# Kernel optimization log

Measured on AMD Instinct MI355X. Metric: run time of the kernel, lower is better.

The kernel has to match this reference:

```python
import jax, jax.numpy as jnp
import numpy as np

THETA = 10000.0
NUM_HEADS = 16
MAX_SEQ_LEN = 2048

def _rope_tables(d_k, max_seq_len, theta=THETA):
    dims = jnp.arange(0, d_k, 2, dtype=jnp.float32)
    freqs = 1.0 / theta ** (dims / d_k)
    t = jnp.arange(max_seq_len, dtype=jnp.float32)
    angles = jnp.outer(t, freqs)  # (max_seq_len, d_k//2)
    return jnp.cos(angles), jnp.sin(angles)

def _apply_rope(x, token_positions, cos_tab, sin_tab):
    # x: (..., seq_len, d_k)
    cos = jnp.repeat(cos_tab[token_positions], 2, axis=-1)  # (seq_len, d_k)
    sin = jnp.repeat(sin_tab[token_positions], 2, axis=-1)
    # interleaved rotate-half: (-x1, x0, -x3, x2, ...)
    xp = x.reshape(*x.shape[:-1], -1, 2)
    x_neg = jnp.stack([-xp[..., 1], xp[..., 0]], axis=-1).reshape(x.shape)
    return x * cos + x_neg * sin

def setup_inputs() -> dict:
    key = jax.random.key(0)
    ks = jax.random.split(key, 5)
    B, S, D = 4, 2048, 1024
    scale = 1.0 / np.sqrt(D)
    return {
        "x": jax.random.normal(ks[0], (B, S, D), dtype=jnp.float32),
        "q_proj": jax.random.normal(ks[1], (D, D), dtype=jnp.float32) * scale,
        "k_proj": jax.random.normal(ks[2], (D, D), dtype=jnp.float32) * scale,
        "v_proj": jax.random.normal(ks[3], (D, D), dtype=jnp.float32) * scale,
        "o_proj": jax.random.normal(ks[4], (D, D), dtype=jnp.float32) * scale,
        "token_positions": jnp.arange(S, dtype=jnp.int64),
    }

def reference(x, q_proj, k_proj, v_proj, o_proj, token_positions):
    B, S, D = x.shape
    H = NUM_HEADS
    d_k = D // H
    cos_tab, sin_tab = _rope_tables(d_k, MAX_SEQ_LEN)

    q = (x @ q_proj).reshape(B, S, H, d_k).transpose(0, 2, 1, 3)  # (B,H,S,d_k)
    k = (x @ k_proj).reshape(B, S, H, d_k).transpose(0, 2, 1, 3)
    v = (x @ v_proj).reshape(B, S, H, d_k).transpose(0, 2, 1, 3)

    q = _apply_rope(q, token_positions, cos_tab, sin_tab)
    k = _apply_rope(k, token_positions, cos_tab, sin_tab)

    scores = jnp.einsum('bhqd,bhkd->bhqk', q, k) / jnp.sqrt(jnp.float32(d_k))
    causal = jnp.tril(jnp.ones((S, S), dtype=bool))
    scores = jnp.where(causal, scores, -jnp.inf)
    attn = jax.nn.softmax(scores, axis=-1)
    out = jnp.einsum('bhqk,bhkd->bhqd', attn, v)  # (B,H,S,d_k)
    out = out.transpose(0, 2, 1, 3).reshape(B, S, D)
    return out @ o_proj
```

## Files before the change

kernel.cpp:

```cpp
#include <hip/hip_runtime.h>
#include <hip/hip_bf16.h>
#include <stdint.h>


typedef __attribute__((ext_vector_type(8))) short short8;
typedef __attribute__((ext_vector_type(4))) float floatx4;
typedef __attribute__((ext_vector_type(16))) float floatx16;

#define MFMA16(a,b,c) __builtin_amdgcn_mfma_f32_16x16x32_bf16((a),(b),(c),0,0,0)
#define MFMA32(a,b,c) __builtin_amdgcn_mfma_f32_32x32x16_bf16((a),(b),(c),0,0,0)

__device__ __forceinline__ uint32_t fbits(float f){ uint32_t u; __builtin_memcpy(&u,&f,4); return u; }
__device__ __forceinline__ unsigned short f2bf(float f) {
    uint32_t u = fbits(f);
    return (unsigned short)((u + 0x7fffu + ((u>>16)&1u)) >> 16);
}
__device__ __forceinline__ float bf2f(unsigned short s){ uint32_t u = (uint32_t)s<<16; float f; __builtin_memcpy(&f,&u,4); return f; }
__device__ __forceinline__ uint32_t pkbf(float lo, float hi) {
#if __has_builtin(__builtin_amdgcn_cvt_pk_bf16_f32)
    auto r = __builtin_amdgcn_cvt_pk_bf16_f32(lo, hi);
    uint32_t u; __builtin_memcpy(&u, &r, sizeof(u));
    return u;
#else
    return __builtin_amdgcn_perm(fbits(hi)+0x8000u, fbits(lo)+0x8000u, 0x07060302u);
#endif
}

__device__ __forceinline__ void load_lds16(const unsigned short* g, unsigned short* l) {
    __builtin_amdgcn_global_load_lds(
        (const __attribute__((address_space(1))) void*)g,
        (__attribute__((address_space(3))) void*)l, 16, 0, 0);
}

__device__ __forceinline__ bool sniff_f32(const unsigned short* xr) {
    int lane = threadIdx.x & 63;
    int bad = 0;
#pragma unroll
    for (int i = 0; i < 16; i++) {
        float v = bf2f(xr[lane * 16 + i]);
        if (!(__builtin_fabsf(v) < 1e10f)) bad = 1;
    }
    return __ballot(bad != 0) != 0ull;
}

__global__ __launch_bounds__(256) void prep_k(
    const void* __restrict__ x,
    const void* __restrict__ wq, const void* __restrict__ wk,
    const void* __restrict__ wv, const void* __restrict__ wo,
    unsigned short* __restrict__ WT, unsigned short* __restrict__ WoT,
    float2* __restrict__ tab, unsigned short* __restrict__ xb) {
    int blk = blockIdx.x, t = threadIdx.x;
    bool f32 = sniff_f32((const unsigned short*)x);
    if (blk < 4096) {
        __shared__ unsigned short tile[32][33];
        int mat = blk >> 10, r = blk & 1023;
        const void* src = (mat == 0) ? wq : (mat == 1) ? wk : (mat == 2) ? wv : wo;
        unsigned short* dst = (mat < 3) ? (WT + (size_t)mat * 1048576) : WoT;
        int bx = (r & 31) * 32, by = (r >> 5) * 32;
        int tx = t & 31, ty = t >> 5;
#pragma unroll
        for (int j = 0; j < 32; j += 8) {
            size_t idx = (size_t)(by + ty + j) * 1024 + bx + tx;
            float v = f32 ? ((const float*)src)[idx] : bf2f(((const unsigned short*)src)[idx]);
            tile[ty + j][tx] = f2bf(v);
        }
        __syncthreads();
#pragma unroll
        for (int j = 0; j < 32; j += 8)
            dst[(size_t)(bx + ty + j) * 1024 + by + tx] = tile[tx][ty + j];
    } else if (blk < 4352) {
        int i = (blk - 4096) * 256 + t;
        int pos = i >> 5, j = i & 31;
        float freq = exp2f(-(float)(2 * j) * (1.0f / 64.0f) * 13.287712379549449f);
        float a = (float)pos * freq;
        tab[i] = make_float2(cosf(a), sinf(a));
    } else {
        size_t base = (size_t)(blk - 4352) * 2048 + (size_t)t * 8;
        if (f32) {
            const float4* s4 = (const float4*)((const float*)x + base);
            float4 a = s4[0], b = s4[1];
            uint4 o;
            o.x = pkbf(a.x, a.y); o.y = pkbf(a.z, a.w);
            o.z = pkbf(b.x, b.y); o.w = pkbf(b.z, b.w);
            *(uint4*)(xb + base) = o;
        } else {
            *(uint4*)(xb + base) = *(const uint4*)((const unsigned short*)x + base);
        }
    }
}

template <int MODE>
__global__ __launch_bounds__(256) void gemm_bt(
    const unsigned short* __restrict__ A,
    const unsigned short* __restrict__ Bt,
    void* __restrict__ C0,
    unsigned short* __restrict__ C1,
    unsigned short* __restrict__ C2,
    const float2* __restrict__ tab,
    const unsigned short* __restrict__ xsniff) {
    const int K = 1024;
    __shared__ __align__(16) unsigned short Al[2][128 * 32];
    __shared__ __align__(16) unsigned short Bl[2][128 * 32];

    int m0 = blockIdx.y * 128;
    int n0 = blockIdx.x * 128;
    int t = threadIdx.x;
    int lane = t & 63, w = t >> 6;
    int quad = lane >> 4, l15 = lane & 15;
    int wm = (w >> 1) * 64, wn = (w & 1) * 64;

    floatx4 acc[4][4];
#pragma unroll
    for (int i = 0; i < 4; i++)
#pragma unroll
        for (int j = 0; j < 4; j++) acc[i][j] = (floatx4){0.f, 0.f, 0.f, 0.f};

    const unsigned short* ag[2];
    const unsigned short* bg[2];
    int lofs[2];
#pragma unroll
    for (int c = 0; c < 2; c++) {
        int row = w * 32 + c * 16 + (lane >> 2);
        ag[c] = A + (size_t)(m0 + row) * K + (lane & 3) * 8;
        bg[c] = Bt + (size_t)(n0 + row) * K + (lane & 3) * 8;
        lofs[c] = (w * 32 + c * 16) * 32;
    }

#pragma unroll
    for (int c = 0; c < 2; c++) {
        load_lds16(ag[c], &Al[0][lofs[c]]);
        load_lds16(bg[c], &Bl[0][lofs[c]]);
        ag[c] += 32; bg[c] += 32;
    }
    asm volatile("s_waitcnt vmcnt(0)" ::: "memory");
    __syncthreads();

    for (int kk = 0; kk < 16; kk++) {
#pragma unroll
        for (int c = 0; c < 2; c++) {
            load_lds16(ag[c], &Al[1][lofs[c]]);
            load_lds16(bg[c], &Bl[1][lofs[c]]);
            ag[c] += 32; bg[c] += 32;
        }
        {
            short8 af[4], bfr[4];
#pragma unroll
            for (int i = 0; i < 4; i++)
                af[i] = *(const short8*)&Al[0][(wm + i * 16 + l15) * 32 + quad * 8];
#pragma unroll
            for (int j = 0; j < 4; j++)
                bfr[j] = *(const short8*)&Bl[0][(wn + j * 16 + l15) * 32 + quad * 8];
#pragma unroll
            for (int i = 0; i < 4; i++)
#pragma unroll
                for (int j = 0; j < 4; j++) acc[i][j] = MFMA16(af[i], bfr[j], acc[i][j]);
        }
        asm volatile("s_waitcnt vmcnt(0)" ::: "memory");
        __syncthreads();

        if (kk < 15) {
#pragma unroll
            for (int c = 0; c < 2; c++) {
                load_lds16(ag[c], &Al[0][lofs[c]]);
                load_lds16(bg[c], &Bl[0][lofs[c]]);
                ag[c] += 32; bg[c] += 32;
            }
        }
        {
            short8 af[4], bfr[4];
#pragma unroll
            for (int i = 0; i < 4; i++)
                af[i] = *(const short8*)&Al[1][(wm + i * 16 + l15) * 32 + quad * 8];
#pragma unroll
            for (int j = 0; j < 4; j++)
                bfr[j] = *(const short8*)&Bl[1][(wn + j * 16 + l15) * 32 + quad * 8];
#pragma unroll
            for (int i = 0; i < 4; i++)
#pragma unroll
                for (int j = 0; j < 4; j++) acc[i][j] = MFMA16(af[i], bfr[j], acc[i][j]);
        }
        asm volatile("s_waitcnt vmcnt(0)" ::: "memory");
        __syncthreads();
    }

    bool out_f32 = (MODE == 0) ? sniff_f32(xsniff) : false;
#pragma unroll
    for (int i = 0; i < 4; i++) {
#pragma unroll
        for (int j = 0; j < 4; j++) {
            int col = n0 + wn + j * 16 + l15;
            int row0 = m0 + wm + i * 16 + quad * 4;
            if (MODE == 0) {
#pragma unroll
                for (int r = 0; r < 4; r++) {
                    size_t idx = (size_t)(row0 + r) * 1024 + col;
                    if (out_f32) ((float*)C0)[idx] = acc[i][j][r];
                    else ((unsigned short*)C0)[idx] = f2bf(acc[i][j][r]);
                }
            } else {
                int which = col >> 10, nn = col & 1023;
                int b = row0 >> 11, s0 = row0 & 2047;
                if (which == 2) {
                    int hh = nn >> 6, d = nn & 63;
                    uint32_t lo = pkbf(acc[i][j][0], acc[i][j][1]);
                    uint32_t hi = pkbf(acc[i][j][2], acc[i][j][3]);
                    *(uint64_t*)(C2 + ((size_t)((b * 16 + hh) * 64 + d)) * 2048 + s0) =
                        (uint64_t)lo | ((uint64_t)hi << 32);
                } else {
                    int d = nn & 63;
                    unsigned short* dst = (which == 0) ? (unsigned short*)C0 : C1;
                    float sc = (which == 0) ? 0.18033688011112042f : 1.0f;
#pragma unroll
                    for (int r = 0; r < 4; r++) {
                        int s = s0 + r;
                        float v = acc[i][j][r];
                        float pv = __shfl_xor(v, 1);
                        float2 cs = tab[(s << 5) + (d >> 1)];
                        float o = (d & 1) ? (v * cs.x + pv * cs.y) : (v * cs.x - pv * cs.y);
                        dst[((size_t)(b * 2048 + s)) * 1024 + nn] = f2bf(o * sc);
                    }
                }
            }
        }
    }
}

__global__ __launch_bounds__(256, 4) void flash_k(
    const unsigned short* __restrict__ Qb,
    const unsigned short* __restrict__ Kb,
    const unsigned short* __restrict__ Vt,
    unsigned short* __restrict__ A2) {
    __shared__ __align__(16) unsigned short Kl[2][64 * 64];
    __shared__ __align__(16) unsigned short Vl[2][64 * 64];

    int bh = blockIdx.x;
    int y = blockIdx.y;
    int qt = (y < 8) ? (15 - y) : (y - 8);
    int b = bh >> 4, h = bh & 15;
    int t = threadIdx.x, lane = t & 63, w = t >> 6;
    int l31 = lane & 31, half = lane >> 5;
    size_t base = ((size_t)b * 2048) * 1024 + h * 64;
    int q0w = qt * 128 + w * 32;

    short8 Qf[4];
#pragma unroll
    for (int ks = 0; ks < 4; ks++)
        Qf[ks] = *(const short8*)(Qb + base + (size_t)(q0w + l31) * 1024 + ks * 16 + half * 8);

    floatx16 O[2];
    O[0] = (floatx16)0.0f; O[1] = (floatx16)0.0f;
    float lsum = 0.f;

    int nk = 2 * (qt + 1);

    int srow = t >> 2;
    const unsigned short* kg = Kb + base + (size_t)srow * 1024 + (t & 3) * 16;
    const unsigned short* vg = Vt + ((size_t)(bh * 64 + srow)) * 2048 + (t & 3) * 16;
    int sw0 = srow * 64 + ((((t & 3) * 2 + 0) ^ (srow & 7)) * 8);
    int sw1 = srow * 64 + ((((t & 3) * 2 + 1) ^ (srow & 7)) * 8);

    short8 rk0 = *(const short8*)(kg);
    short8 rk1 = *(const short8*)(kg + 8);
    short8 rv0 = *(const short8*)(vg);
    short8 rv1 = *(const short8*)(vg + 8);

    for (int kt = 0; kt < nk; kt++) {
        int k0 = kt * 64, bf = kt & 1;
        *(short8*)&Kl[bf][sw0] = rk0;
        *(short8*)&Kl[bf][sw1] = rk1;
        *(short8*)&Vl[bf][sw0] = rv0;
        *(short8*)&Vl[bf][sw1] = rv1;
        __syncthreads();
        if (kt + 1 < nk) {
            size_t ko = (size_t)(kt + 1) * 64;
            rk0 = *(const short8*)(kg + ko * 1024);
            rk1 = *(const short8*)(kg + ko * 1024 + 8);
            rv0 = *(const short8*)(vg + ko);
            rv1 = *(const short8*)(vg + ko + 8);
        }
#pragma unroll
        for (int mb = 0; mb < 2; mb++) {
            if (k0 + mb * 32 >= q0w + 32) continue;
            short8 Ka[4];
#pragma unroll
            for (int ks = 0; ks < 4; ks++)
                Ka[ks] = *(const short8*)&Kl[bf][(mb * 32 + l31) * 64 +
                                                 (((ks * 2 + half) ^ (l31 & 7)) * 8)];
            floatx16 Sc = (floatx16)0.0f;
#pragma unroll
            for (int ks = 0; ks < 4; ks++)
                Sc = MFMA32(Ka[ks], Qf[ks], Sc);

            bool domask = (k0 + mb * 32 + 31 > q0w);
            float p[16];
#pragma unroll
            for (int e = 0; e < 16; e++) {
                float v = exp2f(Sc[e]);
                if (domask) {
                    int kv = k0 + mb * 32 + (e & 3) + ((e >> 2) << 3) + half * 4;
                    int qq = q0w + l31;
                    v = (kv > qq) ? 0.f : v;
                }
                p[e] = v;
            }
            float t0 = (p[0] + p[1]) + (p[2] + p[3]);
            float t1 = (p[4] + p[5]) + (p[6] + p[7]);
            float t2 = (p[8] + p[9]) + (p[10] + p[11]);
            float t3 = (p[12] + p[13]) + (p[14] + p[15]);
            lsum += (t0 + t1) + (t2 + t3);
            uint32_t pkm[8];
#pragma unroll
            for (int jj = 0; jj < 8; jj++)
                pkm[jj] = pkbf(p[2 * jj], p[2 * jj + 1]);

            short8 Va[2][2];
#pragma unroll
            for (int db = 0; db < 2; db++)
#pragma unroll
                for (int ks2 = 0; ks2 < 2; ks2++)
                    Va[db][ks2] = *(const short8*)&Vl[bf][(db * 32 + l31) * 64 +
                                                         ((((mb * 2 + ks2) * 2 + half) ^ (l31 & 7)) * 8)];
#pragma unroll
            for (int ks2 = 0; ks2 < 2; ks2++) {
                uint32_t p0 = pkm[4 * ks2 + 0];
                uint32_t p1 = pkm[4 * ks2 + 1];
                uint32_t p2 = pkm[4 * ks2 + 2];
                uint32_t p3 = pkm[4 * ks2 + 3];
                uint32_t u = half ? p0 : p2;
                uint32_t v2 = half ? p1 : p3;
                uint32_t ya = (uint32_t)__shfl_xor((int)u, 32);
                uint32_t yb = (uint32_t)__shfl_xor((int)v2, 32);
                union { short8 s; uint32_t q[4]; } bb;
                bb.q[0] = half ? ya : p0;
                bb.q[1] = half ? yb : p1;
                bb.q[2] = half ? p2 : ya;
                bb.q[3] = half ? p3 : yb;
#pragma unroll
                for (int db = 0; db < 2; db++)
                    O[db] = MFMA32(Va[db][ks2], bb.s, O[db]);
            }
        }
    }

    float tot = lsum + __shfl_xor(lsum, 32);
    float inv = 1.0f / tot;
#pragma unroll
    for (int db = 0; db < 2; db++) {
        int scol = q0w + l31;
        unsigned short* op = A2 + base + (size_t)scol * 1024;
#pragma unroll
        for (int g = 0; g < 4; g++) {
            int d0 = db * 32 + half * 4 + g * 8;
            float v0 = O[db][g * 4 + 0] * inv;
            float v1 = O[db][g * 4 + 1] * inv;
            float v2 = O[db][g * 4 + 2] * inv;
            float v3 = O[db][g * 4 + 3] * inv;
            uint32_t lo = pkbf(v0, v1), hi = pkbf(v2, v3);
            *(uint64_t*)(op + d0) = (uint64_t)lo | ((uint64_t)hi << 32);
        }
    }
}

extern "C" void kernel_launch(void* const* d_in, const int* in_sizes, int n_in,
                              void* d_out, int out_size, void* d_ws, size_t ws_size,
                              hipStream_t stream) {
    const void* x  = d_in[0];
    const void* wq = d_in[1];
    const void* wk = d_in[2];
    const void* wv = d_in[3];
    const void* wo = d_in[4];

    char* ws = (char*)d_ws;
    unsigned short* WT  = (unsigned short*)(ws);
    unsigned short* WoT = (unsigned short*)(ws + 6291456);
    float2*         tab = (float2*)(ws + 8388608);
    unsigned short* xb  = (unsigned short*)(ws + 8913920);
    unsigned short* Qb  = (unsigned short*)(ws + 8913920 + 16777216ull);
    unsigned short* Kb  = (unsigned short*)(ws + 8913920 + 2ull * 16777216);
    unsigned short* Vt  = (unsigned short*)(ws + 8913920 + 3ull * 16777216);
    unsigned short* A2  = xb;

    prep_k<<<8448, 256, 0, stream>>>(x, wq, wk, wv, wo, WT, WoT, tab, xb);

    gemm_bt<1><<<dim3(24, 64), 256, 0, stream>>>(xb, WT, Qb, Kb, Vt, tab,
                                                 (const unsigned short*)x);
    flash_k<<<dim3(64, 16), 256, 0, stream>>>(Qb, Kb, Vt, A2);
    gemm_bt<0><<<dim3(8, 64), 256, 0, stream>>>(A2, WoT, d_out, nullptr, nullptr, tab,
                                                (const unsigned short*)x);
}
```

Measured before the change: 281.1 us.

## Rewrite projection GEMMs with 8-wave 128x256 tiles and triple-buffered LDS pipeline

Replaces the 256-thread 128x128 double-buffered GEMM with a 512-thread 128x256 tile kernel. It uses BK=64, a three-stage LDS ring in dynamic shared memory, XOR-swizzled LDS layout, and an XCD-aware block index swizzle. Global loads for stage k+2 are interleaved between MFMA phases, with s_setprio raising MFMA priority and partial vmcnt waits. This targets better latency hiding and cache reuse in the QKV and output projections, at the cost of 144KB of LDS per block, which limits occupancy, and more barriers per k-step.

```diff
diff --git a/kernel.cpp b/kernel.cpp
--- a/kernel.cpp
+++ b/kernel.cpp
@@ -9,6 +9,9 @@
 
 #define MFMA16(a,b,c) __builtin_amdgcn_mfma_f32_16x16x32_bf16((a),(b),(c),0,0,0)
 #define MFMA32(a,b,c) __builtin_amdgcn_mfma_f32_32x32x16_bf16((a),(b),(c),0,0,0)
+#define BAR() __builtin_amdgcn_s_barrier()
+#define LGKM0 asm volatile("s_waitcnt lgkmcnt(0)" ::: "memory")
+#define VMCNT6 asm volatile("s_waitcnt vmcnt(6)" ::: "memory")
 
 __device__ __forceinline__ uint32_t fbits(float f){ uint32_t u; __builtin_memcpy(&u,&f,4); return u; }
 __device__ __forceinline__ unsigned short f2bf(float f) {
@@ -90,7 +93,7 @@
 }
 
 template <int MODE>
-__global__ __launch_bounds__(256) void gemm_bt(
+__global__ __launch_bounds__(512, 2) void gemm8(
     const unsigned short* __restrict__ A,
     const unsigned short* __restrict__ Bt,
     void* __restrict__ C0,
@@ -99,15 +102,21 @@
     const float2* __restrict__ tab,
     const unsigned short* __restrict__ xsniff) {
     const int K = 1024;
-    __shared__ __align__(16) unsigned short Al[2][128 * 32];
-    __shared__ __align__(16) unsigned short Bl[2][128 * 32];
-
-    int m0 = blockIdx.y * 128;
-    int n0 = blockIdx.x * 128;
+    extern __shared__ __align__(16) char smraw[];
+    unsigned short* Asm = (unsigned short*)smraw;
+    unsigned short* Bsm = Asm + 3 * 8192;
+
     int t = threadIdx.x;
     int lane = t & 63, w = t >> 6;
     int quad = lane >> 4, l15 = lane & 15;
-    int wm = (w >> 1) * 64, wn = (w & 1) * 64;
+    int wm = (w >> 2) * 64, wn = (w & 3) * 64;
+
+    int nbx = gridDim.x;
+    int flat = blockIdx.y * nbx + blockIdx.x;
+    int cpx = (nbx * gridDim.y) >> 3;
+    int swzid = (flat & 7) * cpx + (flat >> 3);
+    int bx = swzid % nbx, by = swzid / nbx;
+    int m0 = by * 128, n0 = bx * 256;
 
     floatx4 acc[4][4];
 #pragma unroll
@@ -115,72 +124,105 @@
 #pragma unroll
         for (int j = 0; j < 4; j++) acc[i][j] = (floatx4){0.f, 0.f, 0.f, 0.f};
 
-    const unsigned short* ag[2];
-    const unsigned short* bg[2];
-    int lofs[2];
-#pragma unroll
-    for (int c = 0; c < 2; c++) {
-        int row = w * 32 + c * 16 + (lane >> 2);
-        ag[c] = A + (size_t)(m0 + row) * K + (lane & 3) * 8;
-        bg[c] = Bt + (size_t)(n0 + row) * K + (lane & 3) * 8;
-        lofs[c] = (w * 32 + c * 16) * 32;
-    }
-
-#pragma unroll
-    for (int c = 0; c < 2; c++) {
-        load_lds16(ag[c], &Al[0][lofs[c]]);
-        load_lds16(bg[c], &Bl[0][lofs[c]]);
-        ag[c] += 32; bg[c] += 32;
-    }
-    asm volatile("s_waitcnt vmcnt(0)" ::: "memory");
+    int srow = t >> 3;
+    int sg = ((t & 7) ^ (srow & 7)) * 8;
+    const unsigned short* gA = A + (size_t)(m0 + srow) * K + sg;
+    const unsigned short* gB = Bt + (size_t)(n0 + srow) * K + sg;
+    unsigned short* lA = Asm + w * 512;
+    unsigned short* lB = Bsm + w * 512;
+
+    int rA[4], rB[4], ce[2];
+#pragma unroll
+    for (int m = 0; m < 4; m++) rA[m] = (wm + m * 16 + l15) * 64;
+#pragma unroll
+    for (int n = 0; n < 4; n++) rB[n] = (wn + n * 16 + l15) * 64;
+#pragma unroll
+    for (int ks = 0; ks < 2; ks++)
+        ce[ks] = ((ks * 64 + quad * 16) ^ ((l15 & 7) << 4)) >> 1;
+
+#pragma unroll
+    for (int kt = 0; kt < 2; kt++) {
+#pragma unroll
+        for (int h = 0; h < 2; h++)
+            load_lds16(gA + (size_t)h * 64 * K + kt * 64, lA + kt * 8192 + h * 4096);
+#pragma unroll
+        for (int c = 0; c < 4; c++)
+            load_lds16(gB + (size_t)c * 64 * K + kt * 64, lB + kt * 16384 + c * 4096);
+    }
+    VMCNT6;
     __syncthreads();
 
-    for (int kk = 0; kk < 16; kk++) {
-#pragma unroll
-        for (int c = 0; c < 2; c++) {
-            load_lds16(ag[c], &Al[1][lofs[c]]);
-            load_lds16(bg[c], &Bl[1][lofs[c]]);
-            ag[c] += 32; bg[c] += 32;
-        }
-        {
-            short8 af[4], bfr[4];
-#pragma unroll
-            for (int i = 0; i < 4; i++)
-                af[i] = *(const short8*)&Al[0][(wm + i * 16 + l15) * 32 + quad * 8];
-#pragma unroll
-            for (int j = 0; j < 4; j++)
-                bfr[j] = *(const short8*)&Bl[0][(wn + j * 16 + l15) * 32 + quad * 8];
-#pragma unroll
-            for (int i = 0; i < 4; i++)
-#pragma unroll
-                for (int j = 0; j < 4; j++) acc[i][j] = MFMA16(af[i], bfr[j], acc[i][j]);
-        }
-        asm volatile("s_waitcnt vmcnt(0)" ::: "memory");
-        __syncthreads();
-
-        if (kk < 15) {
-#pragma unroll
-            for (int c = 0; c < 2; c++) {
-                load_lds16(ag[c], &Al[0][lofs[c]]);
-                load_lds16(bg[c], &Bl[0][lofs[c]]);
-                ag[c] += 32; bg[c] += 32;
-            }
-        }
-        {
-            short8 af[4], bfr[4];
-#pragma unroll
-            for (int i = 0; i < 4; i++)
-                af[i] = *(const short8*)&Al[1][(wm + i * 16 + l15) * 32 + quad * 8];
-#pragma unroll
-            for (int j = 0; j < 4; j++)
-                bfr[j] = *(const short8*)&Bl[1][(wn + j * 16 + l15) * 32 + quad * 8];
-#pragma unroll
-            for (int i = 0; i < 4; i++)
-#pragma unroll
-                for (int j = 0; j < 4; j++) acc[i][j] = MFMA16(af[i], bfr[j], acc[i][j]);
-        }
-        asm volatile("s_waitcnt vmcnt(0)" ::: "memory");
-        __syncthreads();
+    int cur = 0, nxt = 2;
+#pragma unroll 1
+    for (int kt = 0; kt < 16; kt++) {
+        const unsigned short* cA = Asm + cur * 8192;
+        const unsigned short* cB = Bsm + cur * 16384;
+        unsigned short* nA = lA + nxt * 8192;
+        unsigned short* nB = lB + nxt * 16384;
+        size_t ko = (size_t)(kt + 2) * 64;
+        short8 a0[4], a1[4], bf0, bf1;
+
+#pragma unroll
+        for (int m = 0; m < 4; m++) a0[m] = *(const short8*)(cA + rA[m] + ce[0]);
+        bf0 = *(const short8*)(cB + rB[0] + ce[0]);
+        bf1 = *(const short8*)(cB + rB[1] + ce[0]);
+        load_lds16(gA + ko, nA);
+        load_lds16(gA + (size_t)64 * K + ko, nA + 4096);
+        BAR(); LGKM0;
+        __builtin_amdgcn_s_setprio(1);
+#pragma unroll
+        for (int m = 0; m < 4; m++) {
+            acc[m][0] = MFMA16(a0[m], bf0, acc[m][0]);
+            acc[m][1] = MFMA16(a0[m], bf1, acc[m][1]);
+        }
+        __builtin_amdgcn_s_setprio(0);
+        BAR();
+
+        bf0 = *(const short8*)(cB + rB[2] + ce[0]);
+        bf1 = *(const short8*)(cB + rB[3] + ce[0]);
+        load_lds16(gB + ko, nB);
+        load_lds16(gB + (size_t)64 * K + ko, nB + 4096);
+        BAR(); LGKM0;
+        __builtin_amdgcn_s_setprio(1);
+#pragma unroll
+        for (int m = 0; m < 4; m++) {
+            acc[m][2] = MFMA16(a0[m], bf0, acc[m][2]);
+            acc[m][3] = MFMA16(a0[m], bf1, acc[m][3]);
+        }
+        __builtin_amdgcn_s_setprio(0);
+        BAR();
+
+#pragma unroll
+        for (int m = 0; m < 4; m++) a1[m] = *(const short8*)(cA + rA[m] + ce[1]);
+        bf0 = *(const short8*)(cB + rB[0] + ce[1]);
+        bf1 = *(const short8*)(cB + rB[1] + ce[1]);
+        load_lds16(gB + (size_t)128 * K + ko, nB + 8192);
+        load_lds16(gB + (size_t)192 * K + ko, nB + 12288);
+        BAR(); LGKM0;
+        __builtin_amdgcn_s_setprio(1);
+#pragma unroll
+        for (int m = 0; m < 4; m++) {
+            acc[m][0] = MFMA16(a1[m], bf0, acc[m][0]);
+            acc[m][1] = MFMA16(a1[m], bf1, acc[m][1]);
+        }
+        __builtin_amdgcn_s_setprio(0);
+        BAR();
+
+        bf0 = *(const short8*)(cB + rB[2] + ce[1]);
+        bf1 = *(const short8*)(cB + rB[3] + ce[1]);
+        BAR(); LGKM0;
+        __builtin_amdgcn_s_setprio(1);
+#pragma unroll
+        for (int m = 0; m < 4; m++) {
+            acc[m][2] = MFMA16(a1[m], bf0, acc[m][2]);
+            acc[m][3] = MFMA16(a1[m], bf1, acc[m][3]);
+        }
+        __builtin_amdgcn_s_setprio(0);
+        VMCNT6;
+        BAR();
+
+        cur = (cur == 2) ? 0 : cur + 1;
+        nxt = (nxt == 2) ? 0 : nxt + 1;
     }
 
     bool out_f32 = (MODE == 0) ? sniff_f32(xsniff) : false;
@@ -380,11 +422,16 @@
     unsigned short* Vt  = (unsigned short*)(ws + 8913920 + 3ull * 16777216);
     unsigned short* A2  = xb;
 
+    (void)hipFuncSetAttribute(reinterpret_cast<const void*>(gemm8<1>),
+                              hipFuncAttributeMaxDynamicSharedMemorySize, 147456);
+    (void)hipFuncSetAttribute(reinterpret_cast<const void*>(gemm8<0>),
+                              hipFuncAttributeMaxDynamicSharedMemorySize, 147456);
+
     prep_k<<<8448, 256, 0, stream>>>(x, wq, wk, wv, wo, WT, WoT, tab, xb);
 
-    gemm_bt<1><<<dim3(24, 64), 256, 0, stream>>>(xb, WT, Qb, Kb, Vt, tab,
-                                                 (const unsigned short*)x);
+    gemm8<1><<<dim3(12, 64), 512, 147456, stream>>>(xb, WT, Qb, Kb, Vt, tab,
+                                                    (const unsigned short*)x);
     flash_k<<<dim3(64, 16), 256, 0, stream>>>(Qb, Kb, Vt, A2);
-    gemm_bt<0><<<dim3(8, 64), 256, 0, stream>>>(A2, WoT, d_out, nullptr, nullptr, tab,
-                                                (const unsigned short*)x);
-}
+    gemm8<0><<<dim3(4, 64), 512, 147456, stream>>>(A2, WoT, d_out, nullptr, nullptr, tab,
+                                                   (const unsigned short*)x);
+}
```

New measurement: 256.3 us. -8.8%, faster.
